# Optimization experiments

Hardware: AMD Instinct MI355X
Metric: run time of the kernel (lower is better)

Reference implementation:

```python
import jax, jax.numpy as jnp
import numpy as np

MC_SAMPLES = 32  # k neighbors
BIG = 1e8


def _swish(x):
    return x * jax.nn.sigmoid(x)


def setup_inputs() -> dict:
    key = jax.random.key(0)
    ks = jax.random.split(key, 8)
    bs, n, d, c = 8, 1024, 3, 64
    cmco_ci, hid = 16, 32
    abq_pairs = jax.random.normal(ks[0], (bs, n, n, d), dtype=jnp.float32)
    vals = jax.random.normal(ks[1], (bs, n, c), dtype=jnp.float32)
    mask = jnp.ones((bs, n), dtype=bool)
    s = 0.1
    return {
        "abq_pairs": abq_pairs,
        "vals": vals,
        "mask": mask,
        "W1": jax.random.normal(ks[2], (d, hid), dtype=jnp.float32) * s,
        "b1": jnp.zeros((hid,), jnp.float32),
        "W2": jax.random.normal(ks[3], (hid, hid), dtype=jnp.float32) * s,
        "b2": jnp.zeros((hid,), jnp.float32),
        "W3": jax.random.normal(ks[4], (hid, cmco_ci), dtype=jnp.float32) * s,
        "b3": jnp.zeros((cmco_ci,), jnp.float32),
        "Wl": jax.random.normal(ks[5], (c * cmco_ci, c), dtype=jnp.float32) * s,
        "bl": jnp.zeros((c,), jnp.float32),
    }


def reference(abq_pairs, vals, mask, W1, b1, W2, b2, W3, b3, Wl, bl):
    bs, n, _, d = abq_pairs.shape
    c = vals.shape[-1]
    k = min(MC_SAMPLES, n)

    # --- extract_neighborhood (knn branch, ds_frac=1 so queries = all points) ---
    # Trivial group distance = norm over last dim of abq pairs: (bs,n,n)
    dists = jnp.linalg.norm(abq_pairs, axis=-1)
    dists = jnp.where(mask[:, None, :], dists, BIG)
    _, nbhd_idx = jax.lax.top_k(-dists, k)  # smallest-k -> (bs, n, k)

    # gather neighbor pairwise embeddings: (bs, n, k, d)
    nbhd_abq = jnp.take_along_axis(abq_pairs, nbhd_idx[..., None], axis=2)
    # gather neighbor values and mask per batch: (bs, n, k, c), (bs, n, k)
    nbhd_vals = jax.vmap(lambda v, i: v[i])(vals, nbhd_idx)
    nbhd_mask = jax.vmap(lambda m, i: m[i])(mask, nbhd_idx) & mask[:, :, None]

    h = _swish(nbhd_abq @ W1 + b1)
    h = _swish(h @ W2 + b2)
    penult_kernel_weights = _swish(h @ W3 + b3)  # (bs, n, k, 16)

    # --- masked weighted aggregation (generalized PointConv trick) ---
    mW = jnp.where(nbhd_mask[..., None], penult_kernel_weights, 0.0)
    mV = jnp.where(nbhd_mask[..., None], nbhd_vals, 0.0)
    # vals^T @ weights -> (bs, n, c, 16) -> (bs, n, c*16)
    partial = jnp.einsum("bmkc,bmkp->bmcp", mV, mW).reshape(bs, n, -1)
    convolved = partial @ Wl + bl  # (bs, n, c)

    # zero out invalid query points
    return jnp.where(mask[..., None], convolved, 0.0)
```

## Files before the change

### kernel.cpp

```cpp
#include <hip/hip_runtime.h>
#include <math.h>


#define NPTS 1024
#define KNB  32
#define CCH  64
#define HID  32
#define PCH  16

__device__ __forceinline__ float swishf(float x) {
    return x / (1.0f + __expf(-x));
}

__global__ __launch_bounds__(256, 8) void lieconv_knn(
    const float* __restrict__ abq, unsigned short* __restrict__ sel_out)
{
    __shared__ int s_cand[4][64];
    const int tid  = threadIdx.x;
    const int lane = tid & 63;
    const int w    = tid >> 6;
    const int row  = blockIdx.x * 4 + w;
    const float* __restrict__ rowp = abq + (size_t)row * (NPTS * 3);

    float kf[16];
#pragma unroll
    for (int q = 0; q < 16; ++q) {
        int j = q * 64 + lane;
        float x = rowp[j * 3 + 0];
        float y = rowp[j * 3 + 1];
        float z = rowp[j * 3 + 2];
        kf[q] = fmaf(x, x, fmaf(y, y, z * z));
    }
    float kmax = kf[0];
#pragma unroll
    for (int q = 1; q < 16; ++q) kmax = fmaxf(kmax, kf[q]);
#pragma unroll
    for (int off = 32; off > 0; off >>= 1)
        kmax = fmaxf(kmax, __shfl_xor(kmax, off, 64));

    float lo = 0.0f, hi = kmax * 1.000001f + 1e-30f, T = hi;
    for (int it = 0; it < 28; ++it) {
        float mid = 0.5f * (lo + hi);
        int c = 0;
#pragma unroll
        for (int q = 0; q < 16; ++q)
            c += __popcll(__ballot(kf[q] < mid));
        if (c < KNB)      lo = mid;
        else if (c > 40)  hi = mid;
        else { T = mid; break; }
        T = hi;
    }
    float Tcut = T * 1.000001f;

    const unsigned long long lmask = (1ull << lane) - 1ull;
    int base = 0;
#pragma unroll
    for (int q = 0; q < 16; ++q) {
        bool p = kf[q] < Tcut;
        unsigned long long mk = __ballot(p);
        int pos = base + __popcll(mk & lmask);
        if (p && pos < 64) s_cand[w][pos] = q * 64 + lane;
        base += __popcll(mk);
    }
    int ncand = (base < 64) ? base : 64;

    unsigned long long ci = ~0ull;
    int ji = 0x7fffffff;
    if (lane < ncand) {
        ji = s_cand[w][lane];
        double x = (double)rowp[ji * 3 + 0];
        double y = (double)rowp[ji * 3 + 1];
        double z = (double)rowp[ji * 3 + 2];
        double ki = (x * x + y * y) + z * z;
        ci = ((unsigned long long)__double_as_longlong(ki) & ~1023ull) | (unsigned)ji;
    }
    int rank = 0;
#pragma unroll
    for (int t = 0; t < 64; ++t) {
        unsigned long long ct = __shfl(ci, t, 64);
        rank += (ct < ci) ? 1 : 0;
    }
    bool sel = (lane < ncand) && (rank < KNB);
    unsigned long long mk = __ballot(sel);
    if (sel) sel_out[(size_t)row * KNB + __popcll(mk & lmask)] = (unsigned short)ji;
}

__global__ __launch_bounds__(64, 4) void lieconv_mlp(
    const float* __restrict__ abq, const float* __restrict__ vals,
    const unsigned short* __restrict__ sel_in,
    const float* __restrict__ W1, const float* __restrict__ b1,
    const float* __restrict__ W2, const float* __restrict__ b2,
    const float* __restrict__ W3, const float* __restrict__ b3,
    float* __restrict__ partial)
{
    __shared__ __align__(16) float s_buf[2048];
    __shared__ float s_nb[KNB][3];
    __shared__ int   s_sel[KNB];

    const int lane = threadIdx.x;
    const int row  = blockIdx.x;
    const int b    = row >> 10;
    const float* __restrict__ rowp = abq + (size_t)row * (NPTS * 3);

    if (lane < KNB) {
        int j = (int)sel_in[(size_t)row * KNB + lane];
        s_sel[lane] = j;
        s_nb[lane][0] = rowp[j * 3 + 0];
        s_nb[lane][1] = rowp[j * 3 + 1];
        s_nb[lane][2] = rowp[j * 3 + 2];
    }
    const int o = lane & 31;
    const int p = lane & 15;
    float W1c[3], W2c[32], W3c[32];
#pragma unroll
    for (int e = 0; e < 3; ++e)  W1c[e] = W1[e * HID + o];
#pragma unroll
    for (int ii = 0; ii < 32; ++ii) W2c[ii] = W2[ii * HID + o];
#pragma unroll
    for (int ii = 0; ii < 32; ++ii) W3c[ii] = W3[ii * PCH + p];
    float b1o = b1[o], b2o = b2[o], b3p = b3[p];
    __syncthreads();

    float* bufA = s_buf;
    float* bufB = s_buf + 1024;

    {
        const int kh = lane >> 5;
#pragma unroll
        for (int pass = 0; pass < 16; ++pass) {
            int kk = pass * 2 + kh;
            float acc = b1o;
#pragma unroll
            for (int e = 0; e < 3; ++e) acc = fmaf(s_nb[kk][e], W1c[e], acc);
            bufA[kk * 32 + o] = swishf(acc);
        }
    }
    __syncthreads();

    {
        const int kh = lane >> 5;
#pragma unroll
        for (int pass = 0; pass < 16; ++pass) {
            int kk = pass * 2 + kh;
            float acc = b2o;
            const float4* hrow = (const float4*)&bufA[kk * 32];
#pragma unroll
            for (int i4 = 0; i4 < 8; ++i4) {
                float4 hv = hrow[i4];
                acc = fmaf(hv.x, W2c[i4 * 4 + 0], acc);
                acc = fmaf(hv.y, W2c[i4 * 4 + 1], acc);
                acc = fmaf(hv.z, W2c[i4 * 4 + 2], acc);
                acc = fmaf(hv.w, W2c[i4 * 4 + 3], acc);
            }
            bufB[kk * 32 + o] = swishf(acc);
        }
    }
    __syncthreads();

    float* s_w = s_buf;
    {
        const int k4 = lane >> 4;
#pragma unroll
        for (int pass = 0; pass < 8; ++pass) {
            int kk = pass * 4 + k4;
            float acc = b3p;
            const float4* hrow = (const float4*)&bufB[kk * 32];
#pragma unroll
            for (int i4 = 0; i4 < 8; ++i4) {
                float4 hv = hrow[i4];
                acc = fmaf(hv.x, W3c[i4 * 4 + 0], acc);
                acc = fmaf(hv.y, W3c[i4 * 4 + 1], acc);
                acc = fmaf(hv.z, W3c[i4 * 4 + 2], acc);
                acc = fmaf(hv.w, W3c[i4 * 4 + 3], acc);
            }
            s_w[kk * PCH + p] = swishf(acc);
        }
    }
    __syncthreads();

    const float* __restrict__ valsb = vals + (size_t)b * NPTS * CCH;
    float* chunk = s_buf + 1024;
    const int p4    = (lane & 3) * 4;
    const int cbase = lane >> 2;
    float acc[4][4];
#pragma unroll
    for (int it = 0; it < 4; ++it)
#pragma unroll
        for (int e = 0; e < 4; ++e) acc[it][e] = 0.0f;

    for (int ch = 0; ch < 2; ++ch) {
        __syncthreads();
#pragma unroll
        for (int kk2 = 0; kk2 < 16; ++kk2) {
            int j = s_sel[ch * 16 + kk2];
            chunk[kk2 * 64 + lane] = valsb[(size_t)j * CCH + lane];
        }
        __syncthreads();
#pragma unroll
        for (int kk2 = 0; kk2 < 16; ++kk2) {
            int kk = ch * 16 + kk2;
            float4 wv = *(const float4*)&s_w[kk * PCH + p4];
#pragma unroll
            for (int it = 0; it < 4; ++it) {
                float v = chunk[kk2 * 64 + cbase + 16 * it];
                acc[it][0] = fmaf(v, wv.x, acc[it][0]);
                acc[it][1] = fmaf(v, wv.y, acc[it][1]);
                acc[it][2] = fmaf(v, wv.z, acc[it][2]);
                acc[it][3] = fmaf(v, wv.w, acc[it][3]);
            }
        }
    }

    float* __restrict__ prow = partial + (size_t)row * (CCH * PCH);
#pragma unroll
    for (int it = 0; it < 4; ++it) {
        int c = cbase + 16 * it;
        float4 v = make_float4(acc[it][0], acc[it][1], acc[it][2], acc[it][3]);
        *(float4*)&prow[c * PCH + p4] = v;
    }
}

__global__ __launch_bounds__(256, 4) void lieconv_stage2(
    const float* __restrict__ partial, const float* __restrict__ Wl,
    const float* __restrict__ bl, float* __restrict__ out)
{
    __shared__ __align__(16) float s_part[8][1024];
    const int tid = threadIdx.x;
    const size_t r0 = (size_t)blockIdx.x * 8;

    const float4* gsrc = (const float4*)(partial + r0 * 1024);
    float4* ldst = (float4*)&s_part[0][0];
#pragma unroll
    for (int u = 0; u < 8; ++u) {
        int idx = u * 256 + tid;
        ldst[idx] = gsrc[idx];
    }
    __syncthreads();

    const int c  = tid & 63;
    const int rg = tid >> 6;
    float a0 = 0.0f, a1 = 0.0f;
    for (int k = 0; k < 1024; k += 4) {
        float4 q0 = *(const float4*)&s_part[rg][k];
        float4 q1 = *(const float4*)&s_part[rg + 4][k];
        float w0 = Wl[(size_t)(k + 0) * 64 + c];
        float w1 = Wl[(size_t)(k + 1) * 64 + c];
        float w2 = Wl[(size_t)(k + 2) * 64 + c];
        float w3 = Wl[(size_t)(k + 3) * 64 + c];
        a0 = fmaf(q0.x, w0, a0); a0 = fmaf(q0.y, w1, a0);
        a0 = fmaf(q0.z, w2, a0); a0 = fmaf(q0.w, w3, a0);
        a1 = fmaf(q1.x, w0, a1); a1 = fmaf(q1.y, w1, a1);
        a1 = fmaf(q1.z, w2, a1); a1 = fmaf(q1.w, w3, a1);
    }
    float bc = bl[c];
    out[(r0 + rg) * 64 + c]     = a0 + bc;
    out[(r0 + rg + 4) * 64 + c] = a1 + bc;
}

extern "C" void kernel_launch(void* const* d_in, const int* in_sizes, int n_in,
                              void* d_out, int out_size, void* d_ws, size_t ws_size,
                              hipStream_t stream)
{
    const float* abq  = (const float*)d_in[0];
    const float* vals = (const float*)d_in[1];
    const float* W1 = (const float*)d_in[3];
    const float* b1 = (const float*)d_in[4];
    const float* W2 = (const float*)d_in[5];
    const float* b2 = (const float*)d_in[6];
    const float* W3 = (const float*)d_in[7];
    const float* b3 = (const float*)d_in[8];
    const float* Wl = (const float*)d_in[9];
    const float* bl = (const float*)d_in[10];
    float* out = (float*)d_out;
    float* partial = (float*)d_ws;
    unsigned short* sel = (unsigned short*)d_out;

    hipLaunchKernelGGL(lieconv_knn, dim3(2048), dim3(256), 0, stream, abq, sel);
    hipLaunchKernelGGL(lieconv_mlp, dim3(8192), dim3(64), 0, stream,
                       abq, vals, sel, W1, b1, W2, b2, W3, b3, partial);
    hipLaunchKernelGGL(lieconv_stage2, dim3(1024), dim3(256), 0, stream,
                       partial, Wl, bl, out);
}
```

Baseline: 247.4 us.

## Restructure pipeline: per-neighbor MLP threads, fuse aggregation with final linear

Adds a pack kernel that lays the MLP weights out as float4-friendly blocks and stores Wl transposed. The kNN kernel now also writes the gathered neighbor coordinates. The MLP runs one thread per (row, neighbor) entirely in registers, with no shared-memory syncs between layers. The aggregation is fused with the final linear layer, which drops the large partial buffer round trip through global memory and lets Wl be read as contiguous float4s. The cost is an extra launch, a kernel-weights buffer written to workspace, and heavy register use in the MLP thread.

New measurement: 350.9 us. 1.42x slower.

```diff
diff --git a/kernel.cpp b/kernel.cpp
--- a/kernel.cpp
+++ b/kernel.cpp
@@ -8,12 +8,53 @@
 #define HID  32
 #define PCH  16
 
+#define OFF_WLT   131072
+#define OFF_PACK  196608
+#define OFF_WBUF  262144
+#define OFF_NB    4456448
+
 __device__ __forceinline__ float swishf(float x) {
     return x / (1.0f + __expf(-x));
 }
 
+__global__ __launch_bounds__(256) void lieconv_pack(
+    const float* __restrict__ Wl,
+    const float* __restrict__ W1, const float* __restrict__ b1,
+    const float* __restrict__ W2, const float* __restrict__ b2,
+    const float* __restrict__ W3, const float* __restrict__ b3,
+    float* __restrict__ ws)
+{
+    const int tid = threadIdx.x;
+    if (blockIdx.x < 64) {
+        int c = blockIdx.x;
+        float* WlT = ws + OFF_WLT;
+        for (int k = tid; k < 1024; k += 256)
+            WlT[c * 1024 + k] = Wl[(size_t)k * 64 + c];
+    } else {
+        float* pack = ws + OFF_PACK;
+        for (int idx = tid; idx < 1808; idx += 256) {
+            float v;
+            if (idx < 128) {
+                int i4 = idx >> 4, rem = idx & 15, r = rem >> 2, u = rem & 3;
+                v = (r < 3) ? W1[r * 32 + i4 * 4 + u] : b1[i4 * 4 + u];
+            } else if (idx < 1792) {
+                int oi = idx - 128;
+                int o = oi / 52, t = oi - o * 52;
+                if (t < 32)       v = W2[t * 32 + o];
+                else if (t < 48)  v = W3[o * 16 + (t - 32)];
+                else if (t == 48) v = b2[o];
+                else              v = 0.0f;
+            } else {
+                v = b3[idx - 1792];
+            }
+            pack[idx] = v;
+        }
+    }
+}
+
 __global__ __launch_bounds__(256, 8) void lieconv_knn(
-    const float* __restrict__ abq, unsigned short* __restrict__ sel_out)
+    const float* __restrict__ abq, unsigned short* __restrict__ sel_out,
+    float* __restrict__ nbbuf)
 {
     __shared__ int s_cand[4][64];
     const int tid  = threadIdx.x;
@@ -82,175 +123,143 @@
     }
     bool sel = (lane < ncand) && (rank < KNB);
     unsigned long long mk = __ballot(sel);
-    if (sel) sel_out[(size_t)row * KNB + __popcll(mk & lmask)] = (unsigned short)ji;
-}
-
-__global__ __launch_bounds__(64, 4) void lieconv_mlp(
-    const float* __restrict__ abq, const float* __restrict__ vals,
-    const unsigned short* __restrict__ sel_in,
-    const float* __restrict__ W1, const float* __restrict__ b1,
-    const float* __restrict__ W2, const float* __restrict__ b2,
-    const float* __restrict__ W3, const float* __restrict__ b3,
-    float* __restrict__ partial)
-{
-    __shared__ __align__(16) float s_buf[2048];
-    __shared__ float s_nb[KNB][3];
-    __shared__ int   s_sel[KNB];
-
-    const int lane = threadIdx.x;
-    const int row  = blockIdx.x;
-    const int b    = row >> 10;
-    const float* __restrict__ rowp = abq + (size_t)row * (NPTS * 3);
-
-    if (lane < KNB) {
-        int j = (int)sel_in[(size_t)row * KNB + lane];
-        s_sel[lane] = j;
-        s_nb[lane][0] = rowp[j * 3 + 0];
-        s_nb[lane][1] = rowp[j * 3 + 1];
-        s_nb[lane][2] = rowp[j * 3 + 2];
-    }
-    const int o = lane & 31;
-    const int p = lane & 15;
-    float W1c[3], W2c[32], W3c[32];
-#pragma unroll
-    for (int e = 0; e < 3; ++e)  W1c[e] = W1[e * HID + o];
-#pragma unroll
-    for (int ii = 0; ii < 32; ++ii) W2c[ii] = W2[ii * HID + o];
-#pragma unroll
-    for (int ii = 0; ii < 32; ++ii) W3c[ii] = W3[ii * PCH + p];
-    float b1o = b1[o], b2o = b2[o], b3p = b3[p];
-    __syncthreads();
-
-    float* bufA = s_buf;
-    float* bufB = s_buf + 1024;
-
+    if (sel) {
+        int pos = (int)((size_t)row * KNB) + __popcll(mk & lmask);
+        sel_out[pos] = (unsigned short)ji;
+        float* nb = nbbuf + (size_t)pos * 3;
+        nb[0] = rowp[ji * 3 + 0];
+        nb[1] = rowp[ji * 3 + 1];
+        nb[2] = rowp[ji * 3 + 2];
+    }
+}
+
+__global__ __launch_bounds__(256, 4) void lieconv_mlp(
+    const float* __restrict__ ws_ro, const unsigned short* __restrict__ sel_in,
+    float* __restrict__ wbuf)
+{
+    const int P = blockIdx.x * 256 + threadIdx.x;
+    const float* __restrict__ nb = ws_ro + OFF_NB + (size_t)P * 3;
+    float x = nb[0], y = nb[1], z = nb[2];
+
+    const float4* __restrict__ w1p = (const float4*)(ws_ro + OFF_PACK);
+    const float4* __restrict__ opk = (const float4*)(ws_ro + OFF_PACK) + 32;
+    const float4* __restrict__ b3q = (const float4*)(ws_ro + OFF_PACK + 1792);
+
+    float h1[32];
+#pragma unroll
+    for (int i4 = 0; i4 < 8; ++i4) {
+        float4 qa = w1p[i4 * 4 + 0];
+        float4 qb = w1p[i4 * 4 + 1];
+        float4 qc = w1p[i4 * 4 + 2];
+        float4 qd = w1p[i4 * 4 + 3];
+        h1[i4 * 4 + 0] = swishf(fmaf(x, qa.x, fmaf(y, qb.x, fmaf(z, qc.x, qd.x))));
+        h1[i4 * 4 + 1] = swishf(fmaf(x, qa.y, fmaf(y, qb.y, fmaf(z, qc.y, qd.y))));
+        h1[i4 * 4 + 2] = swishf(fmaf(x, qa.z, fmaf(y, qb.z, fmaf(z, qc.z, qd.z))));
+        h1[i4 * 4 + 3] = swishf(fmaf(x, qa.w, fmaf(y, qb.w, fmaf(z, qc.w, qd.w))));
+    }
+
+    float wv[16];
     {
-        const int kh = lane >> 5;
-#pragma unroll
-        for (int pass = 0; pass < 16; ++pass) {
-            int kk = pass * 2 + kh;
-            float acc = b1o;
-#pragma unroll
-            for (int e = 0; e < 3; ++e) acc = fmaf(s_nb[kk][e], W1c[e], acc);
-            bufA[kk * 32 + o] = swishf(acc);
-        }
-    }
-    __syncthreads();
-
-    {
-        const int kh = lane >> 5;
-#pragma unroll
-        for (int pass = 0; pass < 16; ++pass) {
-            int kk = pass * 2 + kh;
-            float acc = b2o;
-            const float4* hrow = (const float4*)&bufA[kk * 32];
-#pragma unroll
-            for (int i4 = 0; i4 < 8; ++i4) {
-                float4 hv = hrow[i4];
-                acc = fmaf(hv.x, W2c[i4 * 4 + 0], acc);
-                acc = fmaf(hv.y, W2c[i4 * 4 + 1], acc);
-                acc = fmaf(hv.z, W2c[i4 * 4 + 2], acc);
-                acc = fmaf(hv.w, W2c[i4 * 4 + 3], acc);
-            }
-            bufB[kk * 32 + o] = swishf(acc);
-        }
-    }
-    __syncthreads();
-
-    float* s_w = s_buf;
-    {
-        const int k4 = lane >> 4;
-#pragma unroll
-        for (int pass = 0; pass < 8; ++pass) {
-            int kk = pass * 4 + k4;
-            float acc = b3p;
-            const float4* hrow = (const float4*)&bufB[kk * 32];
-#pragma unroll
-            for (int i4 = 0; i4 < 8; ++i4) {
-                float4 hv = hrow[i4];
-                acc = fmaf(hv.x, W3c[i4 * 4 + 0], acc);
-                acc = fmaf(hv.y, W3c[i4 * 4 + 1], acc);
-                acc = fmaf(hv.z, W3c[i4 * 4 + 2], acc);
-                acc = fmaf(hv.w, W3c[i4 * 4 + 3], acc);
-            }
-            s_w[kk * PCH + p] = swishf(acc);
-        }
-    }
-    __syncthreads();
-
-    const float* __restrict__ valsb = vals + (size_t)b * NPTS * CCH;
-    float* chunk = s_buf + 1024;
+        float4 q0 = b3q[0], q1 = b3q[1], q2 = b3q[2], q3 = b3q[3];
+        wv[0]=q0.x; wv[1]=q0.y; wv[2]=q0.z; wv[3]=q0.w;
+        wv[4]=q1.x; wv[5]=q1.y; wv[6]=q1.z; wv[7]=q1.w;
+        wv[8]=q2.x; wv[9]=q2.y; wv[10]=q2.z; wv[11]=q2.w;
+        wv[12]=q3.x; wv[13]=q3.y; wv[14]=q3.z; wv[15]=q3.w;
+    }
+#pragma unroll
+    for (int o = 0; o < 32; ++o) {
+        const float4* q = opk + o * 13;
+        float acc = q[12].x;
+#pragma unroll
+        for (int n = 0; n < 8; ++n) {
+            float4 qq = q[n];
+            acc = fmaf(h1[n * 4 + 0], qq.x, acc);
+            acc = fmaf(h1[n * 4 + 1], qq.y, acc);
+            acc = fmaf(h1[n * 4 + 2], qq.z, acc);
+            acc = fmaf(h1[n * 4 + 3], qq.w, acc);
+        }
+        float h2 = swishf(acc);
+#pragma unroll
+        for (int n = 0; n < 4; ++n) {
+            float4 qq = q[8 + n];
+            wv[n * 4 + 0] = fmaf(h2, qq.x, wv[n * 4 + 0]);
+            wv[n * 4 + 1] = fmaf(h2, qq.y, wv[n * 4 + 1]);
+            wv[n * 4 + 2] = fmaf(h2, qq.z, wv[n * 4 + 2]);
+            wv[n * 4 + 3] = fmaf(h2, qq.w, wv[n * 4 + 3]);
+        }
+    }
+    float4* wo = (float4*)(wbuf + (size_t)P * PCH);
+#pragma unroll
+    for (int n = 0; n < 4; ++n)
+        wo[n] = make_float4(swishf(wv[n * 4 + 0]), swishf(wv[n * 4 + 1]),
+                            swishf(wv[n * 4 + 2]), swishf(wv[n * 4 + 3]));
+    (void)sel_in;
+}
+
+__global__ __launch_bounds__(256, 4) void lieconv_agg(
+    const float* __restrict__ vals, const unsigned short* __restrict__ sel,
+    const float* __restrict__ ws_ro, const float* __restrict__ bl,
+    float* __restrict__ out)
+{
+    __shared__ __align__(16) float s_part[8][1024];
+    const int tid  = threadIdx.x;
+    const int lane = tid & 63;
+    const int w    = tid >> 6;
+    const size_t r0 = (size_t)blockIdx.x * 8;
+
+    const float* __restrict__ wbuf = ws_ro + OFF_WBUF;
     const int p4    = (lane & 3) * 4;
     const int cbase = lane >> 2;
-    float acc[4][4];
-#pragma unroll
-    for (int it = 0; it < 4; ++it)
-#pragma unroll
-        for (int e = 0; e < 4; ++e) acc[it][e] = 0.0f;
-
-    for (int ch = 0; ch < 2; ++ch) {
-        __syncthreads();
-#pragma unroll
-        for (int kk2 = 0; kk2 < 16; ++kk2) {
-            int j = s_sel[ch * 16 + kk2];
-            chunk[kk2 * 64 + lane] = valsb[(size_t)j * CCH + lane];
-        }
-        __syncthreads();
-#pragma unroll
-        for (int kk2 = 0; kk2 < 16; ++kk2) {
-            int kk = ch * 16 + kk2;
-            float4 wv = *(const float4*)&s_w[kk * PCH + p4];
+
+#pragma unroll
+    for (int rr = 0; rr < 2; ++rr) {
+        const int lr = w * 2 + rr;
+        const size_t R = r0 + lr;
+        const float* __restrict__ valsb = vals + (R >> 10) * (size_t)(NPTS * CCH);
+        const float* __restrict__ wrow  = wbuf + R * (KNB * PCH);
+        const unsigned short* __restrict__ selr = sel + R * KNB;
+
+        float acc[4][4];
+#pragma unroll
+        for (int it = 0; it < 4; ++it)
+#pragma unroll
+            for (int e = 0; e < 4; ++e) acc[it][e] = 0.0f;
+
+#pragma unroll 4
+        for (int kk = 0; kk < KNB; ++kk) {
+            int jj = (int)selr[kk];
+            float4 wq = *(const float4*)&wrow[kk * PCH + p4];
+            const float* vr = valsb + (size_t)jj * CCH + cbase;
 #pragma unroll
             for (int it = 0; it < 4; ++it) {
-                float v = chunk[kk2 * 64 + cbase + 16 * it];
-                acc[it][0] = fmaf(v, wv.x, acc[it][0]);
-                acc[it][1] = fmaf(v, wv.y, acc[it][1]);
-                acc[it][2] = fmaf(v, wv.z, acc[it][2]);
-                acc[it][3] = fmaf(v, wv.w, acc[it][3]);
+                float v = vr[16 * it];
+                acc[it][0] = fmaf(v, wq.x, acc[it][0]);
+                acc[it][1] = fmaf(v, wq.y, acc[it][1]);
+                acc[it][2] = fmaf(v, wq.z, acc[it][2]);
+                acc[it][3] = fmaf(v, wq.w, acc[it][3]);
             }
         }
-    }
-
-    float* __restrict__ prow = partial + (size_t)row * (CCH * PCH);
-#pragma unroll
-    for (int it = 0; it < 4; ++it) {
-        int c = cbase + 16 * it;
-        float4 v = make_float4(acc[it][0], acc[it][1], acc[it][2], acc[it][3]);
-        *(float4*)&prow[c * PCH + p4] = v;
-    }
-}
-
-__global__ __launch_bounds__(256, 4) void lieconv_stage2(
-    const float* __restrict__ partial, const float* __restrict__ Wl,
-    const float* __restrict__ bl, float* __restrict__ out)
-{
-    __shared__ __align__(16) float s_part[8][1024];
-    const int tid = threadIdx.x;
-    const size_t r0 = (size_t)blockIdx.x * 8;
-
-    const float4* gsrc = (const float4*)(partial + r0 * 1024);
-    float4* ldst = (float4*)&s_part[0][0];
-#pragma unroll
-    for (int u = 0; u < 8; ++u) {
-        int idx = u * 256 + tid;
-        ldst[idx] = gsrc[idx];
+#pragma unroll
+        for (int it = 0; it < 4; ++it) {
+            int c = cbase + 16 * it;
+            *(float4*)&s_part[lr][c * PCH + p4] =
+                make_float4(acc[it][0], acc[it][1], acc[it][2], acc[it][3]);
+        }
     }
     __syncthreads();
 
-    const int c  = tid & 63;
-    const int rg = tid >> 6;
+    const int c  = lane;
+    const int rg = w;
+    const float* __restrict__ wlc = ws_ro + OFF_WLT + (size_t)c * 1024;
     float a0 = 0.0f, a1 = 0.0f;
     for (int k = 0; k < 1024; k += 4) {
         float4 q0 = *(const float4*)&s_part[rg][k];
         float4 q1 = *(const float4*)&s_part[rg + 4][k];
-        float w0 = Wl[(size_t)(k + 0) * 64 + c];
-        float w1 = Wl[(size_t)(k + 1) * 64 + c];
-        float w2 = Wl[(size_t)(k + 2) * 64 + c];
-        float w3 = Wl[(size_t)(k + 3) * 64 + c];
-        a0 = fmaf(q0.x, w0, a0); a0 = fmaf(q0.y, w1, a0);
-        a0 = fmaf(q0.z, w2, a0); a0 = fmaf(q0.w, w3, a0);
-        a1 = fmaf(q1.x, w0, a1); a1 = fmaf(q1.y, w1, a1);
-        a1 = fmaf(q1.z, w2, a1); a1 = fmaf(q1.w, w3, a1);
+        float4 wq = *(const float4*)&wlc[k];
+        a0 = fmaf(q0.x, wq.x, a0); a0 = fmaf(q0.y, wq.y, a0);
+        a0 = fmaf(q0.z, wq.z, a0); a0 = fmaf(q0.w, wq.w, a0);
+        a1 = fmaf(q1.x, wq.x, a1); a1 = fmaf(q1.y, wq.y, a1);
+        a1 = fmaf(q1.z, wq.z, a1); a1 = fmaf(q1.w, wq.w, a1);
     }
     float bc = bl[c];
     out[(r0 + rg) * 64 + c]     = a0 + bc;
@@ -272,12 +281,18 @@
     const float* Wl = (const float*)d_in[9];
     const float* bl = (const float*)d_in[10];
     float* out = (float*)d_out;
-    float* partial = (float*)d_ws;
-    unsigned short* sel = (unsigned short*)d_out;
-
-    hipLaunchKernelGGL(lieconv_knn, dim3(2048), dim3(256), 0, stream, abq, sel);
-    hipLaunchKernelGGL(lieconv_mlp, dim3(8192), dim3(64), 0, stream,
-                       abq, vals, sel, W1, b1, W2, b2, W3, b3, partial);
-    hipLaunchKernelGGL(lieconv_stage2, dim3(1024), dim3(256), 0, stream,
-                       partial, Wl, bl, out);
-}
+
+    float* ws = (float*)d_ws;
+    unsigned short* sel = (unsigned short*)d_ws;
+    float* nbbuf = ws + OFF_NB;
+    float* wbuf  = ws + OFF_WBUF;
+
+    hipLaunchKernelGGL(lieconv_pack, dim3(65), dim3(256), 0, stream,
+                       Wl, W1, b1, W2, b2, W3, b3, ws);
+    hipLaunchKernelGGL(lieconv_knn, dim3(2048), dim3(256), 0, stream,
+                       abq, sel, nbbuf);
+    hipLaunchKernelGGL(lieconv_mlp, dim3(1024), dim3(256), 0, stream,
+                       ws, sel, wbuf);
+    hipLaunchKernelGGL(lieconv_agg, dim3(1024), dim3(256), 0, stream,
+                       vals, sel, ws, bl, out);
+}
```
